# Performance work log

Hardware: AMD Instinct MI355X
Metric: run time of the kernel (lower is better)

Reference implementation:

```python
import jax, jax.numpy as jnp
import numpy as np
from jax import lax
from jax.scipy.special import ndtr

EV = 6           # even context kernel size
K = 3            # num_mixtures
GROUPS = 3       # grouped 1x1 convs (grps=3 for clrchs<3)
SCALE_MIN = 0.11 # lower bound on mixture std
LP = 257         # 257 CDF sampling points (8-bit Y/RGB path)


def _cdf_pts():
    # cdf_sampling_pts__Y_RGB from __init__
    pts = jnp.linspace(-127.5, 128.5, LP) / 255.0
    pts = pts.at[0].set(-147.5 / 255.0).at[-1].set(148.5 / 255.0)
    return pts.astype(jnp.float32)


def _conv(x, w, b, groups=1):
    y = lax.conv_general_dilated(
        x, w, window_strides=(1, 1), padding='VALID',
        dimension_numbers=('NCHW', 'OIHW', 'NCHW'),
        feature_group_count=groups)
    return y + b[None, :, None, None]


def _forward_float(y_condition, W0, b0, W1, b1, W2, b2):
    # replicate pad: paddd0_00_11 = (Ev//2-1, Ev//2, Ev//2-1, Ev//2)
    y = jnp.pad(y_condition, ((0, 0), (0, 0), (EV // 2 - 1, EV // 2), (EV // 2 - 1, EV // 2)), mode='edge')
    h = jax.nn.relu(_conv(y, W0, b0, groups=1))        # [B, 192, H, W]
    h = jax.nn.relu(_conv(h, W1, b1, groups=GROUPS))   # [B, 192, H, W]
    p = _conv(h, W2, b2, groups=GROUPS)                # [B, 9, H, W] GMM params
    B, _, H, W = p.shape
    p = p.reshape(B, 3, K, H, W)                       # param-major: mu / raw_scale / raw_weight
    mu, sr, wr = p[:, 0], p[:, 1], p[:, 2]             # each [B, K, H, W]
    scale = jnp.maximum(jnp.exp(sr), SCALE_MIN)
    wts = jax.nn.softmax(wr, axis=1)                   # mixture weights over K
    t = _cdf_pts()                                     # [LP]
    z = (t - mu[..., None]) / scale[..., None]         # [B, K, H, W, LP]
    cdf = jnp.einsum('bkhw,bkhwl->bhwl', wts, ndtr(z)) # mixture CDF, [B, H, W, LP]
    return jnp.clip(cdf, 0.0, 1.0 - 1e-6)


def setup_inputs() -> dict:
    key = jax.random.key(0)
    ks = jax.random.split(key, 4)
    return {
        'y_condition': jax.random.uniform(ks[0], (1, 1, 256, 256), jnp.float32),
        'W0': jax.random.normal(ks[1], (192, 1, EV, EV), jnp.float32) * 0.05,
        'b0': jnp.zeros((192,), jnp.float32),
        'W1': jax.random.normal(ks[2], (192, 64, 1, 1), jnp.float32) * 0.05,
        'b1': jnp.zeros((192,), jnp.float32),
        'W2': jax.random.normal(ks[3], (9, 64, 1, 1), jnp.float32) * 0.05,
        'b2': jnp.zeros((9,), jnp.float32),
    }


def reference(y_condition, W0, b0, W1, b1, W2, b2):
    cdf_f = _forward_float(y_condition, W0, b0, W1, b1, W2, b2)
    # _convert_to_int_and_normalize with needs_normalization=True
    new_max = jnp.float32(2 ** 16 - (LP - 1))
    cdf_i = jnp.round(cdf_f * new_max).astype(jnp.int16)
    cdf_i = cdf_i + jnp.arange(LP, dtype=jnp.int16)
    return cdf_i
```

## Files before the change

kernel.cpp:

```cpp
#include <hip/hip_runtime.h>
#include <math.h>

#define LPTS 257
#define NPIX 65536
#define PPB  32


__device__ __forceinline__ float xla_exp32(float x)
{
#pragma clang fp contract(off)
    x = fminf(x, 88.3762626647950f);
    x = fmaxf(x, -87.3365478515625f);
    const float m = floorf(fmaf(x, 1.44269504088896341f, 0.5f));
    float r = fmaf(m, -0.693359375f, x);
    r = fmaf(m, 2.12194440e-4f, r);
    const float r2 = r * r;
    float p = 1.9875691500e-4f;
    p = fmaf(p, r, 1.3981999507e-3f);
    p = fmaf(p, r, 8.3334519073e-3f);
    p = fmaf(p, r, 4.1665795894e-2f);
    p = fmaf(p, r, 1.6666665459e-1f);
    p = fmaf(p, r, 5.0000001201e-1f);
    float y = fmaf(p, r2, r) + 1.0f;
    const int e = (int)m;
    const float s = __int_as_float((e + 127) << 23);
    return y * s;
}

__device__ __forceinline__ float xla_erf32(float x)
{
#pragma clang fp contract(off)
    x = fminf(fmaxf(x, -4.0f), 4.0f);
    const float x2 = x * x;
    float pa = -2.72614225801306e-10f;
    pa = fmaf(pa, x2, 2.77068142495902e-08f);
    pa = fmaf(pa, x2, -2.10102402082508e-06f);
    pa = fmaf(pa, x2, -5.69250639462346e-05f);
    pa = fmaf(pa, x2, -7.34990630326855e-04f);
    pa = fmaf(pa, x2, -2.95459980854025e-03f);
    pa = fmaf(pa, x2, -1.60960333262415e-02f);
    float pb = -1.45660718464996e-05f;
    pb = fmaf(pb, x2, -2.13374055278905e-04f);
    pb = fmaf(pb, x2, -1.68282697438203e-03f);
    pb = fmaf(pb, x2, -7.37332916720468e-03f);
    pb = fmaf(pb, x2, -1.42647390514189e-02f);
    return x * pa / pb;
}

__device__ __forceinline__ float xla_erfc_ge1(float x)
{
#pragma clang fp contract(off)
    const float z = xla_exp32(-(x * x));
    const float q = 1.0f / x;
    const float y2 = q * q;
    float p;
    if (x < 2.0f) {
        p = 2.326819970068386e-02f;
        p = fmaf(p, y2, -1.387039388740657e-01f);
        p = fmaf(p, y2, 3.687424674597105e-01f);
        p = fmaf(p, y2, -5.824733027278666e-01f);
        p = fmaf(p, y2, 6.210004621745983e-01f);
        p = fmaf(p, y2, -4.944515323274145e-01f);
        p = fmaf(p, y2, 3.404879937665872e-01f);
        p = fmaf(p, y2, -2.741127028184656e-01f);
        p = fmaf(p, y2, 5.638259427386472e-01f);
    } else {
        p = -1.047766399936249e+01f;
        p = fmaf(p, y2, 1.297719955372516e+01f);
        p = fmaf(p, y2, -7.495518717768503e+00f);
        p = fmaf(p, y2, 2.921019019210786e+00f);
        p = fmaf(p, y2, -1.015265279202700e+00f);
        p = fmaf(p, y2, 4.218463358204948e-01f);
        p = fmaf(p, y2, -2.820767439740514e-01f);
        p = fmaf(p, y2, 5.641895067754075e-01f);
    }
    return z * q * p;
}

__device__ __forceinline__ float xla_ndtr32(float zf)
{
#pragma clang fp contract(off)
    const float c = __uint_as_float(0x3f3504f3u);
    const float w = zf * c;
    const float aw = fabsf(w);

    const float E = xla_erf32(w);
    const float e_mid = 1.0f - fabsf(E);
    float y = (aw < c) ? (1.0f + E)
                       : ((w > 0.0f) ? (2.0f - e_mid) : e_mid);

    if (__builtin_expect(__ballot(aw > 1.0f) != 0ull, 0)) {
        const float ec = xla_erfc_ge1(aw);
        const float yc = (w > 0.0f) ? (2.0f - ec) : ec;
        y = (aw > 1.0f) ? yc : y;
    }
    return 0.5f * y;
}

__device__ __forceinline__ int quantize(float cdf, int l)
{
    int r = (int)rintf(cdf * 65280.0f);
    r = r > 32767 ? 32767 : r;
    r = r < -32768 ? -32768 : r;
    return (int)((short)(r + l));
}

__global__ __launch_bounds__(256) void entropy_params(
    const float* __restrict__ y,
    const float* __restrict__ W0, const float* __restrict__ b0,
    const float* __restrict__ W1, const float* __restrict__ b1,
    const float* __restrict__ W2, const float* __restrict__ b2,
    float* __restrict__ prm_g)
{
#pragma clang fp contract(off)
    __shared__ float tile[21][22];
    __shared__ __align__(16) float w0s[64 * 36];
    __shared__ __align__(16) float w1s[64 * 64];
    __shared__ __align__(16) float w2s[3 * 64];
    __shared__ __align__(16) float b0s[64];
    __shared__ __align__(16) float b1s[64];
    __shared__ float b2s[3];

    const int bx  = blockIdx.x & 15;
    const int by  = blockIdx.x >> 4;
    const int g   = blockIdx.y;
    const int tid = threadIdx.x;
    const int tx  = tid & 15;
    const int ty  = tid >> 4;

    {
        const float4* src = (const float4*)(W0 + g * 64 * 36);
        for (int i = tid; i < 576; i += 256) ((float4*)w0s)[i] = src[i];
    }
    {
        const float4* src = (const float4*)(W1 + g * 64 * 64);
        for (int i = tid; i < 1024; i += 256) ((float4*)w1s)[i] = src[i];
    }
    {
        const float4* src = (const float4*)(W2 + g * 3 * 64);
        if (tid < 48) ((float4*)w2s)[tid] = src[tid];
    }
    {
        const float4* s0 = (const float4*)(b0 + g * 64);
        const float4* s1 = (const float4*)(b1 + g * 64);
        if (tid < 16)      ((float4*)b0s)[tid]      = s0[tid];
        else if (tid < 32) ((float4*)b1s)[tid - 16] = s1[tid - 16];
        if (tid < 3) b2s[tid] = b2[3 * g + tid];
    }

    for (int idx = tid; idx < 21 * 21; idx += 256) {
        const int r = idx / 21;
        const int c = idx - r * 21;
        int gy = by * 16 - 2 + r; gy = gy < 0 ? 0 : (gy > 255 ? 255 : gy);
        int gx = bx * 16 - 2 + c; gx = gx < 0 ? 0 : (gx > 255 ? 255 : gx);
        tile[r][c] = y[gy * 256 + gx];
    }
    __syncthreads();

    float patch[36];
#pragma unroll
    for (int i = 0; i < 6; ++i)
#pragma unroll
        for (int j = 0; j < 6; ++j)
            patch[i * 6 + j] = tile[ty + i][tx + j];

    float h0[64];
#pragma unroll 4
    for (int c = 0; c < 64; ++c) {
        const float4* w4 = (const float4*)(w0s + c * 36);
        float acc = 0.0f;
#pragma unroll
        for (int q = 0; q < 9; ++q) {
            const float4 wv = w4[q];
            acc = fmaf(wv.x, patch[4 * q + 0], acc);
            acc = fmaf(wv.y, patch[4 * q + 1], acc);
            acc = fmaf(wv.z, patch[4 * q + 2], acc);
            acc = fmaf(wv.w, patch[4 * q + 3], acc);
        }
        acc = acc + b0s[c];
        h0[c] = fmaxf(acc, 0.0f);
    }

    float p0 = 0.0f, p1 = 0.0f, p2 = 0.0f;
#pragma unroll 4
    for (int c = 0; c < 64; ++c) {
        const float4* w4 = (const float4*)(w1s + c * 64);
        float acc = 0.0f;
#pragma unroll
        for (int q = 0; q < 16; ++q) {
            const float4 wv = w4[q];
            acc = fmaf(wv.x, h0[4 * q + 0], acc);
            acc = fmaf(wv.y, h0[4 * q + 1], acc);
            acc = fmaf(wv.z, h0[4 * q + 2], acc);
            acc = fmaf(wv.w, h0[4 * q + 3], acc);
        }
        acc = acc + b1s[c];
        acc = fmaxf(acc, 0.0f);
        p0 = fmaf(w2s[0 * 64 + c], acc, p0);
        p1 = fmaf(w2s[1 * 64 + c], acc, p1);
        p2 = fmaf(w2s[2 * 64 + c], acc, p2);
    }
    p0 = p0 + b2s[0];
    p1 = p1 + b2s[1];
    p2 = p2 + b2s[2];

    const int pix = (by * 16 + ty) * 256 + bx * 16 + tx;

    if (g == 0) {
        prm_g[0 * NPIX + pix] = p0;
        prm_g[1 * NPIX + pix] = p1;
        prm_g[2 * NPIX + pix] = p2;
    } else if (g == 1) {
        prm_g[3 * NPIX + pix] = fmaxf(xla_exp32(p0), 0.11f);
        prm_g[4 * NPIX + pix] = fmaxf(xla_exp32(p1), 0.11f);
        prm_g[5 * NPIX + pix] = fmaxf(xla_exp32(p2), 0.11f);
    } else {
        const float m  = fmaxf(fmaxf(p0, p1), p2);
        const float e0 = xla_exp32(p0 - m);
        const float e1 = xla_exp32(p1 - m);
        const float e2 = xla_exp32(p2 - m);
        const float s  = (e0 + e1) + e2;
        prm_g[6 * NPIX + pix] = e0 / s;
        prm_g[7 * NPIX + pix] = e1 / s;
        prm_g[8 * NPIX + pix] = e2 / s;
    }
}

__global__ __launch_bounds__(256) void entropy_cdf(
    const float* __restrict__ prm_g,
    int* __restrict__ out)
{
#pragma clang fp contract(off)
    __shared__ float prm[9][PPB];

    const int base = blockIdx.x * PPB;
    const int tid  = threadIdx.x;

    for (int i = tid; i < 9 * PPB; i += 256)
        prm[i >> 5][i & 31] = prm_g[(i >> 5) * NPIX + base + (i & 31)];
    __syncthreads();

    const float CLIP = (float)(1.0 - 1e-6);

    {
        const int l = tid;
        const float t32 = (l == 0)
            ? (float)(-147.5 / 255.0)
            : (float)((((double)l) - 127.5) / 255.0);
#pragma unroll 4
        for (int p = 0; p < PPB; ++p) {
            const float mu0 = prm[0][p], mu1 = prm[1][p], mu2 = prm[2][p];
            const float sc0 = prm[3][p], sc1 = prm[4][p], sc2 = prm[5][p];
            const float w0  = prm[6][p], w1  = prm[7][p], w2  = prm[8][p];

            const float n0 = xla_ndtr32((t32 - mu0) / sc0);
            const float n1 = xla_ndtr32((t32 - mu1) / sc1);
            const float n2 = xla_ndtr32((t32 - mu2) / sc2);

            float cdf = fmaf(w2, n2, fmaf(w1, n1, w0 * n0));
            cdf = fminf(fmaxf(cdf, 0.0f), CLIP);

            out[(size_t)(base + p) * LPTS + l] = quantize(cdf, l);
        }
    }

    if (tid < PPB) {
        const int p = tid;
        const float t32 = (float)(148.5 / 255.0);
        const float mu0 = prm[0][p], mu1 = prm[1][p], mu2 = prm[2][p];
        const float sc0 = prm[3][p], sc1 = prm[4][p], sc2 = prm[5][p];
        const float w0  = prm[6][p], w1  = prm[7][p], w2  = prm[8][p];

        const float n0 = xla_ndtr32((t32 - mu0) / sc0);
        const float n1 = xla_ndtr32((t32 - mu1) / sc1);
        const float n2 = xla_ndtr32((t32 - mu2) / sc2);

        float cdf = fmaf(w2, n2, fmaf(w1, n1, w0 * n0));
        cdf = fminf(fmaxf(cdf, 0.0f), CLIP);

        out[(size_t)(base + p) * LPTS + 256] = quantize(cdf, 256);
    }
}

__global__ __launch_bounds__(256) void entropy_fused(
    const float* __restrict__ y,
    const float* __restrict__ W0, const float* __restrict__ b0,
    const float* __restrict__ W1, const float* __restrict__ b1,
    const float* __restrict__ W2, const float* __restrict__ b2,
    int* __restrict__ out)
{
#pragma clang fp contract(off)

    __shared__ float tile[21][22];
    __shared__ float prm[9][257];

    const int bx  = blockIdx.x & 15;
    const int by  = blockIdx.x >> 4;
    const int tid = threadIdx.x;
    const int tx  = tid & 15;
    const int ty  = tid >> 4;

    for (int idx = tid; idx < 21 * 21; idx += 256) {
        const int r = idx / 21;
        const int c = idx - r * 21;
        int gy = by * 16 - 2 + r; gy = gy < 0 ? 0 : (gy > 255 ? 255 : gy);
        int gx = bx * 16 - 2 + c; gx = gx < 0 ? 0 : (gx > 255 ? 255 : gx);
        tile[r][c] = y[gy * 256 + gx];
    }
    __syncthreads();

    float patch[36];
#pragma unroll
    for (int i = 0; i < 6; ++i)
#pragma unroll
        for (int j = 0; j < 6; ++j)
            patch[i * 6 + j] = tile[ty + i][tx + j];

    for (int g = 0; g < 3; ++g) {
        float h0[64];
#pragma unroll 2
        for (int c = 0; c < 64; ++c) {
            float acc = 0.0f;
            const float* w = W0 + (g * 64 + c) * 36;
#pragma unroll
            for (int k = 0; k < 36; ++k)
                acc = fmaf(w[k], patch[k], acc);
            acc = acc + b0[g * 64 + c];
            h0[c] = fmaxf(acc, 0.0f);
        }

        float p0 = 0.0f, p1 = 0.0f, p2 = 0.0f;
#pragma unroll 2
        for (int c = 0; c < 64; ++c) {
            float acc = 0.0f;
            const float* w = W1 + (g * 64 + c) * 64;
#pragma unroll
            for (int j = 0; j < 64; ++j)
                acc = fmaf(w[j], h0[j], acc);
            acc = acc + b1[g * 64 + c];
            acc = fmaxf(acc, 0.0f);
            p0 = fmaf(W2[(3 * g + 0) * 64 + c], acc, p0);
            p1 = fmaf(W2[(3 * g + 1) * 64 + c], acc, p1);
            p2 = fmaf(W2[(3 * g + 2) * 64 + c], acc, p2);
        }
        p0 = p0 + b2[3 * g + 0];
        p1 = p1 + b2[3 * g + 1];
        p2 = p2 + b2[3 * g + 2];

        if (g == 0) {
            prm[0][tid] = p0; prm[1][tid] = p1; prm[2][tid] = p2;
        } else if (g == 1) {
            prm[3][tid] = fmaxf(xla_exp32(p0), 0.11f);
            prm[4][tid] = fmaxf(xla_exp32(p1), 0.11f);
            prm[5][tid] = fmaxf(xla_exp32(p2), 0.11f);
        } else {
            const float m  = fmaxf(fmaxf(p0, p1), p2);
            const float e0 = xla_exp32(p0 - m);
            const float e1 = xla_exp32(p1 - m);
            const float e2 = xla_exp32(p2 - m);
            const float s  = (e0 + e1) + e2;
            prm[6][tid] = e0 / s;
            prm[7][tid] = e1 / s;
            prm[8][tid] = e2 / s;
        }
    }
    __syncthreads();

    const int rowbase = (by * 16) * 256 + bx * 16;
    const float CLIP = (float)(1.0 - 1e-6);

    {
        const int l = tid;
        const float t32 = (l == 0)
            ? (float)(-147.5 / 255.0)
            : (float)((((double)l) - 127.5) / 255.0);
        for (int p = 0; p < 256; ++p) {
            const float mu0 = prm[0][p], mu1 = prm[1][p], mu2 = prm[2][p];
            const float sc0 = prm[3][p], sc1 = prm[4][p], sc2 = prm[5][p];
            const float w0  = prm[6][p], w1  = prm[7][p], w2  = prm[8][p];

            const float n0 = xla_ndtr32((t32 - mu0) / sc0);
            const float n1 = xla_ndtr32((t32 - mu1) / sc1);
            const float n2 = xla_ndtr32((t32 - mu2) / sc2);

            float cdf = fmaf(w2, n2, fmaf(w1, n1, w0 * n0));
            cdf = fminf(fmaxf(cdf, 0.0f), CLIP);

            const int pix = rowbase + (p >> 4) * 256 + (p & 15);
            out[(size_t)pix * LPTS + l] = quantize(cdf, l);
        }
    }

    {
        const int p = tid;
        const float t32 = (float)(148.5 / 255.0);
        const float mu0 = prm[0][p], mu1 = prm[1][p], mu2 = prm[2][p];
        const float sc0 = prm[3][p], sc1 = prm[4][p], sc2 = prm[5][p];
        const float w0  = prm[6][p], w1  = prm[7][p], w2  = prm[8][p];

        const float n0 = xla_ndtr32((t32 - mu0) / sc0);
        const float n1 = xla_ndtr32((t32 - mu1) / sc1);
        const float n2 = xla_ndtr32((t32 - mu2) / sc2);

        float cdf = fmaf(w2, n2, fmaf(w1, n1, w0 * n0));
        cdf = fminf(fmaxf(cdf, 0.0f), CLIP);

        const int pix = rowbase + (p >> 4) * 256 + (p & 15);
        out[(size_t)pix * LPTS + 256] = quantize(cdf, 256);
    }
}

extern "C" void kernel_launch(void* const* d_in, const int* in_sizes, int n_in,
                              void* d_out, int out_size, void* d_ws, size_t ws_size,
                              hipStream_t stream)
{
    const float* y  = (const float*)d_in[0];
    const float* W0 = (const float*)d_in[1];
    const float* b0 = (const float*)d_in[2];
    const float* W1 = (const float*)d_in[3];
    const float* b1 = (const float*)d_in[4];
    const float* W2 = (const float*)d_in[5];
    const float* b2 = (const float*)d_in[6];

    int* out = (int*)d_out;

    const size_t need = (size_t)9 * NPIX * sizeof(float);
    if (d_ws != nullptr && ws_size >= need) {
        float* prm_g = (float*)d_ws;
        entropy_params<<<dim3(256, 3), dim3(256), 0, stream>>>(
            y, W0, b0, W1, b1, W2, b2, prm_g);
        entropy_cdf<<<dim3(NPIX / PPB), dim3(256), 0, stream>>>(prm_g, out);
    } else {
        entropy_fused<<<dim3(256), dim3(256), 0, stream>>>(
            y, W0, b0, W1, b1, W2, b2, out);
    }
}
```

Measured before the change: 202.4 us.

## Precompute reciprocal scales and half-weights, vectorize param loads, batch ndtr

The params kernel now also stores reciprocal scales and mixture weights pre-multiplied by 0.5, in a 12-plane workspace. The CDF kernel reads each pixel's 12 values as three float4 LDS loads and replaces the division by scale with a reciprocal multiply plus one residual correction. It evaluates the three ndtr calls together under a single wave-wide ballot for the erfc branch. The erf division uses a custom rcp-plus-Newton routine, and launch bounds gain occupancy hints. The rounding behaviour is meant to match IEEE division, but the corrected-reciprocal path can differ in the last bit, which would change quantized outputs.

```diff
diff --git a/kernel.cpp b/kernel.cpp
--- a/kernel.cpp
+++ b/kernel.cpp
@@ -27,6 +27,18 @@
     return y * s;
 }
 
+__device__ __forceinline__ float ieee_div(float n, float d)
+{
+    const float r0 = __builtin_amdgcn_rcpf(d);
+    const float e  = fmaf(-d, r0, 1.0f);
+    const float r1 = fmaf(e, r0, r0);
+    const float q0 = n * r1;
+    const float e1 = fmaf(-d, q0, n);
+    const float q1 = fmaf(e1, r1, q0);
+    const float e2 = fmaf(-d, q1, n);
+    return fmaf(e2, r1, q1);
+}
+
 __device__ __forceinline__ float xla_erf32(float x)
 {
 #pragma clang fp contract(off)
@@ -44,7 +56,7 @@
     pb = fmaf(pb, x2, -1.68282697438203e-03f);
     pb = fmaf(pb, x2, -7.37332916720468e-03f);
     pb = fmaf(pb, x2, -1.42647390514189e-02f);
-    return x * pa / pb;
+    return ieee_div(x * pa, pb);
 }
 
 __device__ __forceinline__ float xla_erfc_ge1(float x)
@@ -77,18 +89,57 @@
     return z * q * p;
 }
 
+__device__ __forceinline__ void xla_ndtr3_y(
+    float z0, float z1, float z2, float& o0, float& o1, float& o2)
+{
+#pragma clang fp contract(off)
+    const float c = __uint_as_float(0x3f3504f3u);
+    const float w0 = z0 * c, w1 = z1 * c, w2 = z2 * c;
+    const float a0 = fabsf(w0), a1 = fabsf(w1), a2 = fabsf(w2);
+
+    const float E0 = xla_erf32(w0);
+    const float E1 = xla_erf32(w1);
+    const float E2 = xla_erf32(w2);
+
+    const float m0 = 1.0f - fabsf(E0);
+    const float m1 = 1.0f - fabsf(E1);
+    const float m2 = 1.0f - fabsf(E2);
+
+    float y0 = (a0 < c) ? (1.0f + E0) : ((w0 > 0.0f) ? (2.0f - m0) : m0);
+    float y1 = (a1 < c) ? (1.0f + E1) : ((w1 > 0.0f) ? (2.0f - m1) : m1);
+    float y2 = (a2 < c) ? (1.0f + E2) : ((w2 > 0.0f) ? (2.0f - m2) : m2);
+
+    const float amax = fmaxf(fmaxf(a0, a1), a2);
+    if (__builtin_expect(__ballot(amax > 1.0f) != 0ull, 0)) {
+        {
+            const float ec = xla_erfc_ge1(a0);
+            const float yc = (w0 > 0.0f) ? (2.0f - ec) : ec;
+            y0 = (a0 > 1.0f) ? yc : y0;
+        }
+        {
+            const float ec = xla_erfc_ge1(a1);
+            const float yc = (w1 > 0.0f) ? (2.0f - ec) : ec;
+            y1 = (a1 > 1.0f) ? yc : y1;
+        }
+        {
+            const float ec = xla_erfc_ge1(a2);
+            const float yc = (w2 > 0.0f) ? (2.0f - ec) : ec;
+            y2 = (a2 > 1.0f) ? yc : y2;
+        }
+    }
+    o0 = y0; o1 = y1; o2 = y2;
+}
+
 __device__ __forceinline__ float xla_ndtr32(float zf)
 {
 #pragma clang fp contract(off)
     const float c = __uint_as_float(0x3f3504f3u);
     const float w = zf * c;
     const float aw = fabsf(w);
-
     const float E = xla_erf32(w);
     const float e_mid = 1.0f - fabsf(E);
     float y = (aw < c) ? (1.0f + E)
                        : ((w > 0.0f) ? (2.0f - e_mid) : e_mid);
-
     if (__builtin_expect(__ballot(aw > 1.0f) != 0ull, 0)) {
         const float ec = xla_erfc_ge1(aw);
         const float yc = (w > 0.0f) ? (2.0f - ec) : ec;
@@ -105,7 +156,7 @@
     return (int)((short)(r + l));
 }
 
-__global__ __launch_bounds__(256) void entropy_params(
+__global__ __launch_bounds__(256, 2) void entropy_params(
     const float* __restrict__ y,
     const float* __restrict__ W0, const float* __restrict__ b0,
     const float* __restrict__ W1, const float* __restrict__ b1,
@@ -211,33 +262,42 @@
         prm_g[1 * NPIX + pix] = p1;
         prm_g[2 * NPIX + pix] = p2;
     } else if (g == 1) {
-        prm_g[3 * NPIX + pix] = fmaxf(xla_exp32(p0), 0.11f);
-        prm_g[4 * NPIX + pix] = fmaxf(xla_exp32(p1), 0.11f);
-        prm_g[5 * NPIX + pix] = fmaxf(xla_exp32(p2), 0.11f);
+        const float s0 = fmaxf(xla_exp32(p0), 0.11f);
+        const float s1 = fmaxf(xla_exp32(p1), 0.11f);
+        const float s2 = fmaxf(xla_exp32(p2), 0.11f);
+        prm_g[3 * NPIX + pix] = s0;
+        prm_g[4 * NPIX + pix] = s1;
+        prm_g[5 * NPIX + pix] = s2;
+        prm_g[6 * NPIX + pix] = 1.0f / s0;
+        prm_g[7 * NPIX + pix] = 1.0f / s1;
+        prm_g[8 * NPIX + pix] = 1.0f / s2;
     } else {
         const float m  = fmaxf(fmaxf(p0, p1), p2);
         const float e0 = xla_exp32(p0 - m);
         const float e1 = xla_exp32(p1 - m);
         const float e2 = xla_exp32(p2 - m);
         const float s  = (e0 + e1) + e2;
-        prm_g[6 * NPIX + pix] = e0 / s;
-        prm_g[7 * NPIX + pix] = e1 / s;
-        prm_g[8 * NPIX + pix] = e2 / s;
-    }
-}
-
-__global__ __launch_bounds__(256) void entropy_cdf(
+        prm_g[ 9 * NPIX + pix] = 0.5f * (e0 / s);
+        prm_g[10 * NPIX + pix] = 0.5f * (e1 / s);
+        prm_g[11 * NPIX + pix] = 0.5f * (e2 / s);
+    }
+}
+
+__global__ __launch_bounds__(256, 4) void entropy_cdf(
     const float* __restrict__ prm_g,
     int* __restrict__ out)
 {
 #pragma clang fp contract(off)
-    __shared__ float prm[9][PPB];
+    __shared__ __align__(16) float prm[PPB][12];
 
     const int base = blockIdx.x * PPB;
     const int tid  = threadIdx.x;
 
-    for (int i = tid; i < 9 * PPB; i += 256)
-        prm[i >> 5][i & 31] = prm_g[(i >> 5) * NPIX + base + (i & 31)];
+    for (int i = tid; i < 12 * PPB; i += 256) {
+        const int j = i >> 5;
+        const int p = i & 31;
+        prm[p][j] = prm_g[j * NPIX + base + p];
+    }
     __syncthreads();
 
     const float CLIP = (float)(1.0 - 1e-6);
@@ -249,15 +309,27 @@
             : (float)((((double)l) - 127.5) / 255.0);
 #pragma unroll 4
         for (int p = 0; p < PPB; ++p) {
-            const float mu0 = prm[0][p], mu1 = prm[1][p], mu2 = prm[2][p];
-            const float sc0 = prm[3][p], sc1 = prm[4][p], sc2 = prm[5][p];
-            const float w0  = prm[6][p], w1  = prm[7][p], w2  = prm[8][p];
-
-            const float n0 = xla_ndtr32((t32 - mu0) / sc0);
-            const float n1 = xla_ndtr32((t32 - mu1) / sc1);
-            const float n2 = xla_ndtr32((t32 - mu2) / sc2);
-
-            float cdf = fmaf(w2, n2, fmaf(w1, n1, w0 * n0));
+            const float4 v0 = *(const float4*)&prm[p][0];
+            const float4 v1 = *(const float4*)&prm[p][4];
+            const float4 v2 = *(const float4*)&prm[p][8];
+
+            const float x0 = t32 - v0.x;
+            const float x1 = t32 - v0.y;
+            const float x2 = t32 - v0.z;
+            const float qa = x0 * v1.z;
+            const float qb = x1 * v1.w;
+            const float qc = x2 * v2.x;
+            const float ra = fmaf(-v0.w, qa, x0);
+            const float rb = fmaf(-v1.x, qb, x1);
+            const float rc = fmaf(-v1.y, qc, x2);
+            const float z0 = fmaf(ra, v1.z, qa);
+            const float z1 = fmaf(rb, v1.w, qb);
+            const float z2 = fmaf(rc, v2.x, qc);
+
+            float y0, y1, y2;
+            xla_ndtr3_y(z0, z1, z2, y0, y1, y2);
+
+            float cdf = fmaf(v2.w, y2, fmaf(v2.z, y1, v2.y * y0));
             cdf = fminf(fmaxf(cdf, 0.0f), CLIP);
 
             out[(size_t)(base + p) * LPTS + l] = quantize(cdf, l);
@@ -267,15 +339,27 @@
     if (tid < PPB) {
         const int p = tid;
         const float t32 = (float)(148.5 / 255.0);
-        const float mu0 = prm[0][p], mu1 = prm[1][p], mu2 = prm[2][p];
-        const float sc0 = prm[3][p], sc1 = prm[4][p], sc2 = prm[5][p];
-        const float w0  = prm[6][p], w1  = prm[7][p], w2  = prm[8][p];
-
-        const float n0 = xla_ndtr32((t32 - mu0) / sc0);
-        const float n1 = xla_ndtr32((t32 - mu1) / sc1);
-        const float n2 = xla_ndtr32((t32 - mu2) / sc2);
-
-        float cdf = fmaf(w2, n2, fmaf(w1, n1, w0 * n0));
+        const float4 v0 = *(const float4*)&prm[p][0];
+        const float4 v1 = *(const float4*)&prm[p][4];
+        const float4 v2 = *(const float4*)&prm[p][8];
+
+        const float x0 = t32 - v0.x;
+        const float x1 = t32 - v0.y;
+        const float x2 = t32 - v0.z;
+        const float qa = x0 * v1.z;
+        const float qb = x1 * v1.w;
+        const float qc = x2 * v2.x;
+        const float ra = fmaf(-v0.w, qa, x0);
+        const float rb = fmaf(-v1.x, qb, x1);
+        const float rc = fmaf(-v1.y, qc, x2);
+        const float z0 = fmaf(ra, v1.z, qa);
+        const float z1 = fmaf(rb, v1.w, qb);
+        const float z2 = fmaf(rc, v2.x, qc);
+
+        float y0, y1, y2;
+        xla_ndtr3_y(z0, z1, z2, y0, y1, y2);
+
+        float cdf = fmaf(v2.w, y2, fmaf(v2.z, y1, v2.y * y0));
         cdf = fminf(fmaxf(cdf, 0.0f), CLIP);
 
         out[(size_t)(base + p) * LPTS + 256] = quantize(cdf, 256);
@@ -424,7 +508,7 @@
 
     int* out = (int*)d_out;
 
-    const size_t need = (size_t)9 * NPIX * sizeof(float);
+    const size_t need = (size_t)12 * NPIX * sizeof(float);
     if (d_ws != nullptr && ws_size >= need) {
         float* prm_g = (float*)d_ws;
         entropy_params<<<dim3(256, 3), dim3(256), 0, stream>>>(
```

Result: faster. 177.7 us (-12.2%).
